# Performance work log

Hardware: AMD Instinct MI355X
Metric: run time of the kernel (lower is better)

The kernel has to match this reference:

```python
import jax, jax.numpy as jnp
import numpy as np

B, T, C = 8, 1024, 1024
NH, HD = 16, 64          # num_heads, head_dim (C = NH*HD)
NL = 8                   # num_layers
TPB = 64                 # tokens_per_block (block_causal)
EPS = 1e-5


def setup_inputs() -> dict:
    key = jax.random.key(0)
    ks = jax.random.split(key, 12)
    s = 0.02
    sequences = jax.random.normal(ks[0], (B, T, C), dtype=jnp.float32)
    # block-causal mask: causal OR same-block (tril | block_diag)
    idx = jnp.arange(T)
    mask = (idx[:, None] >= idx[None, :]) | ((idx[:, None] // TPB) == (idx[None, :] // TPB))
    # stacked per-layer params; torch Linear convention: W has shape [out, in]
    d = {
        "sequences": sequences,
        "mask": mask,
        "Wq": jax.random.normal(ks[1], (NL, C, C)) * s, "bq": jnp.zeros((NL, C)),
        "Wk": jax.random.normal(ks[2], (NL, C, C)) * s, "bk": jnp.zeros((NL, C)),
        "Wv": jax.random.normal(ks[3], (NL, C, C)) * s, "bv": jnp.zeros((NL, C)),
        "Wo": jax.random.normal(ks[4], (NL, C, C)) * s, "bo": jnp.zeros((NL, C)),
        "ln1w": jnp.ones((NL, C)), "ln1b": jnp.zeros((NL, C)),
        "ln2w": jnp.ones((NL, C)), "ln2b": jnp.zeros((NL, C)),
        "W1": jax.random.normal(ks[5], (NL, 4 * C, C)) * s, "b1": jnp.zeros((NL, 4 * C)),
        "W2": jax.random.normal(ks[6], (NL, C, 4 * C)) * s, "b2": jnp.zeros((NL, C)),
        "lnfw": jnp.ones((C,)), "lnfb": jnp.zeros((C,)),
    }
    return d


def _layernorm(x, w, b):
    m = jnp.mean(x, axis=-1, keepdims=True)
    v = jnp.mean(jnp.square(x - m), axis=-1, keepdims=True)
    return (x - m) * jax.lax.rsqrt(v + EPS) * w + b


def _linear(x, W, b):  # x: [..., in], W: [out, in]
    return jnp.einsum('...i,oi->...o', x, W) + b


def _attention(h, mask, Wq, bq, Wk, bk, Wv, bv, Wo, bo):
    # h: [B,T,C]
    q = _linear(h, Wq, bq).reshape(B, T, NH, HD)
    k = _linear(h, Wk, bk).reshape(B, T, NH, HD)
    v = _linear(h, Wv, bv).reshape(B, T, NH, HD)
    att = jnp.einsum('bqhd,bkhd->bhqk', q, k) * (HD ** -0.5)
    att = jnp.where(mask, att, -jnp.inf)
    att = jax.nn.softmax(att, axis=-1)
    y = jnp.einsum('bhqk,bkhd->bqhd', att, v).reshape(B, T, C)
    return _linear(y, Wo, bo)


def reference(sequences, mask, Wq, bq, Wk, bk, Wv, bv, Wo, bo,
              ln1w, ln1b, ln2w, ln2b, W1, b1, W2, b2, lnfw, lnfb):
    x = sequences  # dropout p=0
    for i in range(NL):
        h = _layernorm(x, ln1w[i], ln1b[i])
        x = x + _attention(h, mask, Wq[i], bq[i], Wk[i], bk[i], Wv[i], bv[i], Wo[i], bo[i])
        h = _layernorm(x, ln2w[i], ln2b[i])
        h = _linear(h, W1[i], b1[i])
        h = jax.nn.gelu(h, approximate=False)  # torch nn.GELU default = exact erf
        x = x + _linear(h, W2[i], b2[i])
    return _layernorm(x, lnfw, lnfb)
```

## Files before the change

### kernel.cpp

```cpp
#include <hip/hip_runtime.h>
#include <math.h>

typedef unsigned short ushort_t;
typedef __attribute__((ext_vector_type(4))) float f32x4;
typedef __attribute__((ext_vector_type(8))) short short8;

constexpr int BATCH = 8, T = 1024, C = 1024, NH = 16, HD = 64, NL = 8;
constexpr int MROWS = BATCH * T;
constexpr int CS = 3 * C;

#define WAITVM(n) asm volatile("s_waitcnt vmcnt(" #n ")" ::: "memory")
#define WAITLGKM0 asm volatile("s_waitcnt lgkmcnt(0)" ::: "memory")

__device__ __forceinline__ ushort_t f2bf(float f) {
  unsigned u = __builtin_bit_cast(unsigned, f);
  u += 0x7fffu + ((u >> 16) & 1u);
  return (ushort_t)(u >> 16);
}

__device__ __forceinline__ void gload_lds16(const ushort_t* g, ushort_t* l) {
  __builtin_amdgcn_global_load_lds(
      (const __attribute__((address_space(1))) unsigned int*)g,
      (__attribute__((address_space(3))) unsigned int*)l, 16, 0, 0);
}

__global__ __launch_bounds__(256, 8)
void convw_kernel(const float* __restrict__ Wq, const float* __restrict__ Wk,
                  const float* __restrict__ Wv, const float* __restrict__ Wo,
                  const float* __restrict__ W1, const float* __restrict__ W2,
                  const float* __restrict__ bq, const float* __restrict__ bk,
                  const float* __restrict__ bv,
                  ushort_t* __restrict__ wqkv, ushort_t* __restrict__ wo,
                  ushort_t* __restrict__ w1, ushort_t* __restrict__ w2,
                  float* __restrict__ bqkv)
{
  if (blockIdx.x == 6144) {
    int t = threadIdx.x;
    if (t < 384) {
      const float* s = (t < 128) ? (bq + t * 8)
                     : (t < 256) ? (bk + (t - 128) * 8)
                                 : (bv + (t - 256) * 8);
      f32x4 a = ((const f32x4*)s)[0], b = ((const f32x4*)s)[1];
      ((f32x4*)(bqkv + t * 8))[0] = a;
      ((f32x4*)(bqkv + t * 8))[1] = b;
    }
    return;
  }
  int g = blockIdx.x * 256 + threadIdx.x;
  const float* src;
  ushort_t* dst;
  if (g < 393216) {
    int which = g >> 17;
    int r = g & 131071;
    src = (which == 0 ? Wq : which == 1 ? Wk : Wv) + (size_t)r * 8;
    dst = wqkv + (size_t)g * 8;
  } else if (g < 524288) {
    int r = g - 393216;
    src = Wo + (size_t)r * 8; dst = wo + (size_t)r * 8;
  } else if (g < 1048576) {
    int r = g - 524288;
    src = W1 + (size_t)r * 8; dst = w1 + (size_t)r * 8;
  } else {
    int r = g - 1048576;
    src = W2 + (size_t)r * 8; dst = w2 + (size_t)r * 8;
  }
  f32x4 a = ((const f32x4*)src)[0], b = ((const f32x4*)src)[1];
  short8 o;
#pragma unroll
  for (int e = 0; e < 4; ++e) { o[e] = (short)f2bf(a[e]); o[e + 4] = (short)f2bf(b[e]); }
  *(short8*)dst = o;
}

template<int MODE>
__global__ __launch_bounds__(256, 3)
void gemm97(const ushort_t* __restrict__ A, const ushort_t* __restrict__ Wb,
            const float* __restrict__ bias, ushort_t* __restrict__ outb,
            float* __restrict__ resid, int K, int N, int nbn)
{
  __shared__ __align__(16) ushort_t Sm[2 * 128 * 64];
  ushort_t* As = Sm;
  ushort_t* Bs = Sm + 128 * 64;

  const int tid = threadIdx.x;
  const int lane = tid & 63, wave = tid >> 6;
  const int wm = wave >> 1, wn = wave & 1;
  const int l15 = lane & 15, l4 = lane >> 4;

  const int xcd = blockIdx.x & 7;
  const int local = blockIdx.x >> 3;
  const int bm = xcd * 8 + local / nbn;
  const int bn = local % nbn;
  const long bm0 = (long)bm * 128;
  const long bn0 = (long)bn * 128;

  const ushort_t* srcA[4]; const ushort_t* srcB[4]; int dst4[4];
#pragma unroll
  for (int j = 0; j < 4; ++j) {
    int cidx = j * 256 + tid;
    int row = cidx >> 3;
    int cl = (cidx & 7) ^ (row & 7);
    srcA[j] = A + (size_t)(bm0 + row) * K + cl * 8;
    srcB[j] = Wb + (size_t)(bn0 + row) * K + cl * 8;
    dst4[j] = cidx * 8;
  }
  int aoff[2][4], boff[2][4];
#pragma unroll
  for (int ks = 0; ks < 2; ++ks) {
#pragma unroll
    for (int i = 0; i < 4; ++i) {
      int ra = wm * 64 + i * 16 + l15;
      aoff[ks][i] = ra * 64 + (((ks * 4 + l4) ^ (ra & 7)) << 3);
      int rb = wn * 64 + i * 16 + l15;
      boff[ks][i] = rb * 64 + (((ks * 4 + l4) ^ (rb & 7)) << 3);
    }
  }

  f32x4 acc[4][4] = {};
  const int nt = K >> 6;

  for (int t = 0; t < nt; ++t) {
    __syncthreads();
    const int kt = t << 6;
#pragma unroll
    for (int j = 0; j < 4; ++j) {
      gload_lds16(srcA[j] + kt, &As[dst4[j]]);
      gload_lds16(srcB[j] + kt, &Bs[dst4[j]]);
    }
    __syncthreads();
#pragma unroll
    for (int ks = 0; ks < 2; ++ks) {
      short8 af[4], bfr[4];
#pragma unroll
      for (int i = 0; i < 4; ++i) {
        af[i] = *(const short8*)&As[aoff[ks][i]];
        bfr[i] = *(const short8*)&Bs[boff[ks][i]];
      }
#pragma unroll
      for (int mi = 0; mi < 4; ++mi)
#pragma unroll
        for (int ni = 0; ni < 4; ++ni)
          acc[mi][ni] = __builtin_amdgcn_mfma_f32_16x16x32_bf16(
              af[mi], bfr[ni], acc[mi][ni], 0, 0, 0);
    }
  }
  __syncthreads();

  float* fl = (float*)Sm + wave * (16 * 68);
  const long grow0 = bm0 + wm * 64;
  const long gcol0 = bn0 + wn * 64;
  const int c8 = lane & 7;
  const f32x4 bb0 = *(const f32x4*)&bias[gcol0 + c8 * 8];
  const f32x4 bb1 = *(const f32x4*)&bias[gcol0 + c8 * 8 + 4];

#pragma unroll
  for (int mi = 0; mi < 4; ++mi) {
#pragma unroll
    for (int ni = 0; ni < 4; ++ni)
#pragma unroll
      for (int r = 0; r < 4; ++r)
        fl[(l4 * 4 + r) * 68 + ni * 16 + l15] = acc[mi][ni][r];
#pragma unroll
    for (int pass = 0; pass < 2; ++pass) {
      int row = pass * 8 + (lane >> 3);
      f32x4 v0 = *(const f32x4*)&fl[row * 68 + c8 * 8];
      f32x4 v1 = *(const f32x4*)&fl[row * 68 + c8 * 8 + 4];
      v0 += bb0; v1 += bb1;
      const long grow = grow0 + mi * 16 + row;
      if (MODE == 1) {
#pragma unroll
        for (int e = 0; e < 4; ++e) {
          v0[e] = 0.5f * v0[e] * (1.0f + erff(v0[e] * 0.70710678118f));
          v1[e] = 0.5f * v1[e] * (1.0f + erff(v1[e] * 0.70710678118f));
        }
      }
      if (MODE == 2) {
        float* rp = resid + (size_t)grow * N + gcol0 + c8 * 8;
        f32x4 r0 = *(const f32x4*)rp;
        f32x4 r1 = *(const f32x4*)(rp + 4);
        r0 += v0; r1 += v1;
        *(f32x4*)rp = r0;
        *(f32x4*)(rp + 4) = r1;
      } else {
        short8 o;
#pragma unroll
        for (int e = 0; e < 4; ++e) { o[e] = (short)f2bf(v0[e]); o[e + 4] = (short)f2bf(v1[e]); }
        *(short8*)&outb[(size_t)grow * N + gcol0 + c8 * 8] = o;
      }
    }
  }
}

__global__ __launch_bounds__(256, 4)
void attn_kernel(const ushort_t* __restrict__ qkv, ushort_t* __restrict__ y)
{
  __shared__ __align__(16) ushort_t Ks[2][64 * 64];
  __shared__ __align__(16) ushort_t Vts[2][64 * 64];
  __shared__ __align__(16) ushort_t Ps[64 * 64];
  const int tid = threadIdx.x;
  const int lane = tid & 63, wave = tid >> 6;
  const int l15 = lane & 15, l4 = lane >> 4;
  const int w16 = wave * 16;
  const int bh = blockIdx.x & 127, qpair = blockIdx.x >> 7;
  const int h = bh & 15, b = bh >> 4;
  const int qoff = h * HD, koff = C + h * HD, voff = 2 * C + h * HD;
  const int kvr = tid & 63, dc = tid >> 6;

#pragma unroll
  for (int half = 0; half < 2; ++half) {
    const int qb = half == 0 ? qpair : 15 - qpair;
    const int nkv = qb + 1;
    const size_t qrow0 = (size_t)(b * T + qb * 64);

    short8 aq[2];
#pragma unroll
    for (int ks = 0; ks < 2; ++ks)
      aq[ks] = *(const short8*)(qkv + (qrow0 + w16 + l15) * CS + qoff + ks * 32 + l4 * 8);

    f32x4 o[4] = {};
    float mrun[4] = {-INFINITY, -INFINITY, -INFINITY, -INFINITY};
    float lrun[4] = {0.f, 0.f, 0.f, 0.f};

    {
      const size_t krow0 = (size_t)(b * T);
#pragma unroll
      for (int j = 0; j < 2; ++j) {
        int cidx = j * 256 + tid;
        int row = cidx >> 3, cl = (cidx & 7) ^ (row & 7);
        gload_lds16(qkv + (krow0 + row) * CS + koff + cl * 8, &Ks[0][cidx * 8]);
      }
    }
    short8 vreg0, vreg1;
    vreg0 = *(const short8*)(qkv + ((size_t)(b * T) + kvr) * CS + voff + dc * 8);
    vreg1 = *(const short8*)(qkv + ((size_t)(b * T) + kvr) * CS + voff + (dc + 4) * 8);
    WAITVM(2);
    __builtin_amdgcn_s_barrier();

    for (int t = 0; t < nkv; ++t) {
      const int buf = t & 1;
      const bool more = (t + 1 < nkv);
      short8 vnext0, vnext1;
      if (more) {
        const size_t krow1 = (size_t)(b * T + (t + 1) * 64);
#pragma unroll
        for (int j = 0; j < 2; ++j) {
          int cidx = j * 256 + tid;
          int row = cidx >> 3, cl = (cidx & 7) ^ (row & 7);
          gload_lds16(qkv + (krow1 + row) * CS + koff + cl * 8, &Ks[buf ^ 1][cidx * 8]);
        }
        vnext0 = *(const short8*)(qkv + (krow1 + kvr) * CS + voff + dc * 8);
        vnext1 = *(const short8*)(qkv + (krow1 + kvr) * CS + voff + (dc + 4) * 8);
      }

      f32x4 s[4] = {};
#pragma unroll
      for (int ks = 0; ks < 2; ++ks) {
#pragma unroll
        for (int n = 0; n < 4; ++n) {
          int br = n * 16 + l15;
          int pb = (ks * 4 + l4) ^ (br & 7);
          short8 bk2 = *(const short8*)&Ks[buf][br * 64 + pb * 8];
          s[n] = __builtin_amdgcn_mfma_f32_16x16x32_bf16(aq[ks], bk2, s[n], 0, 0, 0);
        }
      }

#pragma unroll
      for (int r = 0; r < 4; ++r) {
        float mx = fmaxf(fmaxf(s[0][r], s[1][r]), fmaxf(s[2][r], s[3][r]));
#pragma unroll
        for (int d = 1; d < 16; d <<= 1) mx = fmaxf(mx, __shfl_xor(mx, d, 16));
        mx *= 0.125f;
        float mnew = fmaxf(mrun[r], mx);
        float alpha = __expf(mrun[r] - mnew);
        float rowsum = 0.f;
        int qr = w16 + l4 * 4 + r;
#pragma unroll
        for (int n = 0; n < 4; ++n) {
          float pv = __expf(s[n][r] * 0.125f - mnew);
          rowsum += pv;
          int kv = n * 16 + l15;
          Ps[qr * 64 + (((kv >> 3) ^ (qr & 7)) << 3) + (kv & 7)] = f2bf(pv);
        }
#pragma unroll
        for (int d = 1; d < 16; d <<= 1) rowsum += __shfl_xor(rowsum, d, 16);
        mrun[r] = mnew;
        lrun[r] = lrun[r] * alpha + rowsum;
        o[0][r] *= alpha; o[1][r] *= alpha; o[2][r] *= alpha; o[3][r] *= alpha;
      }

#pragma unroll
      for (int i = 0; i < 8; ++i) {
        int d0 = dc * 8 + i;
        Vts[buf][d0 * 64 + (((kvr >> 3) ^ (d0 & 7)) << 3) + (kvr & 7)] = (ushort_t)vreg0[i];
        int d1 = (dc + 4) * 8 + i;
        Vts[buf][d1 * 64 + (((kvr >> 3) ^ (d1 & 7)) << 3) + (kvr & 7)] = (ushort_t)vreg1[i];
      }
      vreg0 = vnext0; vreg1 = vnext1;

      WAITLGKM0;
      __builtin_amdgcn_s_barrier();

#pragma unroll
      for (int ks = 0; ks < 2; ++ks) {
        int arow = w16 + l15;
        int pa = (ks * 4 + l4) ^ (arow & 7);
        short8 ap = *(const short8*)&Ps[arow * 64 + pa * 8];
#pragma unroll
        for (int n = 0; n < 4; ++n) {
          int vr = n * 16 + l15;
          int pb = (ks * 4 + l4) ^ (vr & 7);
          short8 bvv = *(const short8*)&Vts[buf][vr * 64 + pb * 8];
          o[n] = __builtin_amdgcn_mfma_f32_16x16x32_bf16(ap, bvv, o[n], 0, 0, 0);
        }
      }

      if (more) { WAITVM(2); }
      __builtin_amdgcn_s_barrier();
    }

#pragma unroll
    for (int n = 0; n < 4; ++n) {
#pragma unroll
      for (int r = 0; r < 4; ++r) {
        float val = o[n][r] / lrun[r];
        y[(qrow0 + w16 + l4 * 4 + r) * C + h * HD + n * 16 + l15] = f2bf(val);
      }
    }
    __builtin_amdgcn_s_barrier();
  }
}

template<int OUTBF16>
__global__ __launch_bounds__(256, 4)
void ln_kernel(const float* __restrict__ x, const float* __restrict__ w,
               const float* __restrict__ bprm, void* __restrict__ out)
{
  const size_t row = blockIdx.x;
  const int tid = threadIdx.x;
  f32x4 xv = ((const f32x4*)(x + row * 1024))[tid];
  float s1 = xv[0] + xv[1] + xv[2] + xv[3];
  float s2 = xv[0] * xv[0] + xv[1] * xv[1] + xv[2] * xv[2] + xv[3] * xv[3];
#pragma unroll
  for (int m = 1; m < 64; m <<= 1) {
    s1 += __shfl_xor(s1, m);
    s2 += __shfl_xor(s2, m);
  }
  __shared__ float red[8];
  const int wave = tid >> 6, lane = tid & 63;
  if (lane == 0) { red[wave * 2] = s1; red[wave * 2 + 1] = s2; }
  __syncthreads();
  s1 = red[0] + red[2] + red[4] + red[6];
  s2 = red[1] + red[3] + red[5] + red[7];
  const float mean = s1 * (1.f / 1024.f);
  const float var = s2 * (1.f / 1024.f) - mean * mean;
  const float rstd = rsqrtf(var + 1e-5f);
  f32x4 wv = ((const f32x4*)w)[tid];
  f32x4 bv = ((const f32x4*)bprm)[tid];
  f32x4 ov;
#pragma unroll
  for (int c2 = 0; c2 < 4; ++c2) ov[c2] = (xv[c2] - mean) * rstd * wv[c2] + bv[c2];
  if (OUTBF16) {
    ushort4 u;
    u.x = f2bf(ov[0]); u.y = f2bf(ov[1]); u.z = f2bf(ov[2]); u.w = f2bf(ov[3]);
    ((ushort4*)out)[row * 256 + tid] = u;
  } else {
    ((f32x4*)out)[row * 256 + tid] = ov;
  }
}

extern "C" void kernel_launch(void* const* d_in, const int* in_sizes, int n_in,
                              void* d_out, int out_size, void* d_ws, size_t ws_size,
                              hipStream_t stream)
{
  const float* seq  = (const float*)d_in[0];
  const float* Wq   = (const float*)d_in[2];  const float* bq = (const float*)d_in[3];
  const float* Wk   = (const float*)d_in[4];  const float* bk = (const float*)d_in[5];
  const float* Wv   = (const float*)d_in[6];  const float* bv = (const float*)d_in[7];
  const float* Wo   = (const float*)d_in[8];  const float* bo = (const float*)d_in[9];
  const float* ln1w = (const float*)d_in[10]; const float* ln1b = (const float*)d_in[11];
  const float* ln2w = (const float*)d_in[12]; const float* ln2b = (const float*)d_in[13];
  const float* W1   = (const float*)d_in[14]; const float* b1 = (const float*)d_in[15];
  const float* W2   = (const float*)d_in[16]; const float* b2 = (const float*)d_in[17];
  const float* lnfw = (const float*)d_in[18]; const float* lnfb = (const float*)d_in[19];

  char* ws = (char*)d_ws;
  size_t off = 0;
  float* X = (float*)(ws + off);         off += (size_t)MROWS * C * 4;
  ushort_t* Hb = (ushort_t*)(ws + off);  off += (size_t)MROWS * C * 2;
  ushort_t* Yb = (ushort_t*)(ws + off);  off += (size_t)MROWS * C * 2;
  ushort_t* BIG = (ushort_t*)(ws + off); off += (size_t)MROWS * 4 * C * 2;
  ushort_t* wqkv = (ushort_t*)(ws + off); off += (size_t)3 * C * C * 2;
  ushort_t* wo   = (ushort_t*)(ws + off); off += (size_t)C * C * 2;
  ushort_t* w1   = (ushort_t*)(ws + off); off += (size_t)4 * C * C * 2;
  ushort_t* w2   = (ushort_t*)(ws + off); off += (size_t)4 * C * C * 2;
  float* bqkv = (float*)(ws + off);       off += (size_t)3 * C * 4;
  ushort_t* QKVb = BIG;
  ushort_t* Gb = BIG;

  hipMemcpyAsync(X, seq, (size_t)MROWS * C * 4, hipMemcpyDeviceToDevice, stream);

  const dim3 blk(256);
  const dim3 gQKV(1536);
  const dim3 gWo(512);
  const dim3 gW1(2048);
  const dim3 gW2(512);
  const dim3 gAttn(1024);
  const dim3 gConv(6145);

  for (int i = 0; i < NL; ++i) {
    const size_t w1Off = (size_t)i * C * C;
    const size_t w4Off = (size_t)i * 4 * C * C;
    convw_kernel<<<gConv, blk, 0, stream>>>(Wq + w1Off, Wk + w1Off, Wv + w1Off,
                                            Wo + w1Off, W1 + w4Off, W2 + w4Off,
                                            bq + i * C, bk + i * C, bv + i * C,
                                            wqkv, wo, w1, w2, bqkv);
    ln_kernel<1><<<MROWS, blk, 0, stream>>>(X, ln1w + i * C, ln1b + i * C, Hb);
    gemm97<0><<<gQKV, blk, 0, stream>>>(Hb, wqkv, bqkv, QKVb, nullptr, C, CS, 24);
    attn_kernel<<<gAttn, blk, 0, stream>>>(QKVb, Yb);
    gemm97<2><<<gWo, blk, 0, stream>>>(Yb, wo, bo + i * C, nullptr, X, C, C, 8);
    ln_kernel<1><<<MROWS, blk, 0, stream>>>(X, ln2w + i * C, ln2b + i * C, Hb);
    gemm97<1><<<gW1, blk, 0, stream>>>(Hb, w1, b1 + (size_t)i * 4 * C, Gb, nullptr, C, 4 * C, 32);
    gemm97<2><<<gW2, blk, 0, stream>>>(Gb, w2, b2 + i * C, nullptr, X, 4 * C, C, 8);
  }
  ln_kernel<0><<<MROWS, blk, 0, stream>>>(X, lnfw, lnfb, (float*)d_out);
}
```

Baseline: 2.926 ms.

## Double-buffer A tile in LDS and load B fragments directly from global

The GEMM kernel now stages only the activation tile in LDS, double-buffered so the next tile's global-to-LDS load overlaps the current MFMA work, and it drops one barrier per k-step. Weight fragments are read straight from global memory into registers and are no longer staged through shared memory. This cuts LDS traffic and synchronisation but makes weight reads uncoalesced, strided per-lane global loads with no sharing between the two waves that use the same columns, which may raise memory latency and cache pressure.

```diff
diff --git a/kernel.cpp b/kernel.cpp
--- a/kernel.cpp
+++ b/kernel.cpp
@@ -73,13 +73,11 @@
 
 template<int MODE>
 __global__ __launch_bounds__(256, 3)
-void gemm97(const ushort_t* __restrict__ A, const ushort_t* __restrict__ Wb,
-            const float* __restrict__ bias, ushort_t* __restrict__ outb,
-            float* __restrict__ resid, int K, int N, int nbn)
+void gemm_bg(const ushort_t* __restrict__ A, const ushort_t* __restrict__ Wb,
+             const float* __restrict__ bias, ushort_t* __restrict__ outb,
+             float* __restrict__ resid, int K, int N, int nbn)
 {
-  __shared__ __align__(16) ushort_t Sm[2 * 128 * 64];
-  ushort_t* As = Sm;
-  ushort_t* Bs = Sm + 128 * 64;
+  __shared__ __align__(16) ushort_t As[2][128 * 64];
 
   const int tid = threadIdx.x;
   const int lane = tid & 63, wave = tid >> 6;
@@ -93,59 +91,64 @@
   const long bm0 = (long)bm * 128;
   const long bn0 = (long)bn * 128;
 
-  const ushort_t* srcA[4]; const ushort_t* srcB[4]; int dst4[4];
+  const ushort_t* srcA[4]; int dstA[4];
 #pragma unroll
   for (int j = 0; j < 4; ++j) {
     int cidx = j * 256 + tid;
     int row = cidx >> 3;
     int cl = (cidx & 7) ^ (row & 7);
     srcA[j] = A + (size_t)(bm0 + row) * K + cl * 8;
-    srcB[j] = Wb + (size_t)(bn0 + row) * K + cl * 8;
-    dst4[j] = cidx * 8;
-  }
-  int aoff[2][4], boff[2][4];
-#pragma unroll
-  for (int ks = 0; ks < 2; ++ks) {
+    dstA[j] = cidx * 8;
+  }
+  int aoff[2][4];
+#pragma unroll
+  for (int ks = 0; ks < 2; ++ks)
 #pragma unroll
     for (int i = 0; i < 4; ++i) {
       int ra = wm * 64 + i * 16 + l15;
       aoff[ks][i] = ra * 64 + (((ks * 4 + l4) ^ (ra & 7)) << 3);
-      int rb = wn * 64 + i * 16 + l15;
-      boff[ks][i] = rb * 64 + (((ks * 4 + l4) ^ (rb & 7)) << 3);
-    }
-  }
+    }
+  const ushort_t* srcBf[4];
+#pragma unroll
+  for (int ni = 0; ni < 4; ++ni)
+    srcBf[ni] = Wb + (size_t)(bn0 + wn * 64 + ni * 16 + l15) * K + l4 * 8;
 
   f32x4 acc[4][4] = {};
   const int nt = K >> 6;
 
+#pragma unroll
+  for (int j = 0; j < 4; ++j) gload_lds16(srcA[j], &As[0][dstA[j]]);
+
   for (int t = 0; t < nt; ++t) {
+    const int buf = t & 1;
+    WAITVM(0);
     __syncthreads();
+    const int kt1 = (t + 1) << 6;
+    if (t + 1 < nt) {
+#pragma unroll
+      for (int j = 0; j < 4; ++j) gload_lds16(srcA[j] + kt1, &As[buf ^ 1][dstA[j]]);
+    }
     const int kt = t << 6;
-#pragma unroll
-    for (int j = 0; j < 4; ++j) {
-      gload_lds16(srcA[j] + kt, &As[dst4[j]]);
-      gload_lds16(srcB[j] + kt, &Bs[dst4[j]]);
-    }
-    __syncthreads();
-#pragma unroll
-    for (int ks = 0; ks < 2; ++ks) {
-      short8 af[4], bfr[4];
+    short8 af[2][4], bfr[2][4];
+#pragma unroll
+    for (int ks = 0; ks < 2; ++ks)
 #pragma unroll
       for (int i = 0; i < 4; ++i) {
-        af[i] = *(const short8*)&As[aoff[ks][i]];
-        bfr[i] = *(const short8*)&Bs[boff[ks][i]];
-      }
+        af[ks][i] = *(const short8*)&As[buf][aoff[ks][i]];
+        bfr[ks][i] = *(const short8*)(srcBf[i] + kt + ks * 32);
+      }
+#pragma unroll
+    for (int ks = 0; ks < 2; ++ks)
 #pragma unroll
       for (int mi = 0; mi < 4; ++mi)
 #pragma unroll
         for (int ni = 0; ni < 4; ++ni)
           acc[mi][ni] = __builtin_amdgcn_mfma_f32_16x16x32_bf16(
-              af[mi], bfr[ni], acc[mi][ni], 0, 0, 0);
-    }
+              af[ks][mi], bfr[ks][ni], acc[mi][ni], 0, 0, 0);
   }
   __syncthreads();
 
-  float* fl = (float*)Sm + wave * (16 * 68);
+  float* fl = (float*)&As[0][0] + wave * (16 * 68);
   const long grow0 = bm0 + wm * 64;
   const long gcol0 = bn0 + wn * 64;
   const int c8 = lane & 7;
@@ -414,12 +417,12 @@
                                             bq + i * C, bk + i * C, bv + i * C,
                                             wqkv, wo, w1, w2, bqkv);
     ln_kernel<1><<<MROWS, blk, 0, stream>>>(X, ln1w + i * C, ln1b + i * C, Hb);
-    gemm97<0><<<gQKV, blk, 0, stream>>>(Hb, wqkv, bqkv, QKVb, nullptr, C, CS, 24);
+    gemm_bg<0><<<gQKV, blk, 0, stream>>>(Hb, wqkv, bqkv, QKVb, nullptr, C, CS, 24);
     attn_kernel<<<gAttn, blk, 0, stream>>>(QKVb, Yb);
-    gemm97<2><<<gWo, blk, 0, stream>>>(Yb, wo, bo + i * C, nullptr, X, C, C, 8);
+    gemm_bg<2><<<gWo, blk, 0, stream>>>(Yb, wo, bo + i * C, nullptr, X, C, C, 8);
     ln_kernel<1><<<MROWS, blk, 0, stream>>>(X, ln2w + i * C, ln2b + i * C, Hb);
-    gemm97<1><<<gW1, blk, 0, stream>>>(Hb, w1, b1 + (size_t)i * 4 * C, Gb, nullptr, C, 4 * C, 32);
-    gemm97<2><<<gW2, blk, 0, stream>>>(Gb, w2, b2 + i * C, nullptr, X, 4 * C, C, 8);
+    gemm_bg<1><<<gW1, blk, 0, stream>>>(Hb, w1, b1 + (size_t)i * 4 * C, Gb, nullptr, C, 4 * C, 32);
+    gemm_bg<2><<<gW2, blk, 0, stream>>>(Gb, w2, b2 + i * C, nullptr, X, 4 * C, C, 8);
   }
   ln_kernel<0><<<MROWS, blk, 0, stream>>>(X, lnfw, lnfb, (float*)d_out);
 }
```

Result: slower. 4.307 ms (+47.2%).
